# Kernel tuning notes

Measured on AMD Instinct MI355X. Metric: run time of the kernel, lower is better.

The kernel has to match this reference:

```python
import jax, jax.numpy as jnp
import numpy as np

B, S, D = 4, 512, 128


def setup_inputs() -> dict:
    key = jax.random.key(0)
    ks = jax.random.split(key, 9)
    scale = 1.0 / np.sqrt(D)
    return {
        "inputs": jax.random.normal(ks[0], (B, S, D), dtype=jnp.float32),
        "encoder_outputs": jax.random.normal(ks[1], (B, S, D), dtype=jnp.float32),
        "mask": jax.random.randint(ks[2], (B, S), 0, 2, dtype=jnp.int32),
        "W1": jax.random.uniform(ks[3], (D, D), jnp.float32, -scale, scale),
        "b1": jax.random.uniform(ks[4], (D,), jnp.float32, -scale, scale),
        "W2": jax.random.uniform(ks[5], (D, D), jnp.float32, -scale, scale),
        "b2": jax.random.uniform(ks[6], (D,), jnp.float32, -scale, scale),
        "v_w": jax.random.uniform(ks[7], (D,), jnp.float32, -scale, scale),
        "v_b": jax.random.uniform(ks[8], (1,), jnp.float32, -scale, scale),
    }


def reference(inputs, encoder_outputs, mask, W1, b1, W2, b2, v_w, v_b):
    # key_out: W1(encoder_outputs)  [B, S_k, D]
    key_out = jnp.einsum("bkd,de->bke", encoder_outputs, W1) + b1
    # query_out: W2(inputs)        [B, S_q, D]
    query_out = jnp.einsum("bqd,de->bqe", inputs, W2) + b2
    # additive attention, all query positions at once: [B, S_q, S_k, D]
    t = jnp.tanh(key_out[:, None, :, :] + query_out[:, :, None, :])
    ui = jnp.einsum("bqkd,d->bqk", t, v_w) + v_b[0]
    # mask out padded key positions for every query position
    valid = mask.astype(bool)[:, None, :]  # [B, 1, S_k]
    logits = jnp.where(valid, ui, -jnp.inf)
    preds = jnp.argmax(logits, axis=-1)
    return (logits, preds)
```

## Files before the change

kernel.cpp:

```cpp
#include <hip/hip_runtime.h>
#include <math.h>

#define NB 4
#define NS 512
#define ND 128

static constexpr float K2LE = 2.885390081777927f;

__device__ inline float fast_exp2(float x){
#if __has_builtin(__builtin_amdgcn_exp2f)
  return __builtin_amdgcn_exp2f(x);
#else
  float r; asm("v_exp_f32 %0, %1" : "=v"(r) : "v"(x)); return r;
#endif
}
__device__ inline float fast_rcp(float x){
#if __has_builtin(__builtin_amdgcn_rcpf)
  return __builtin_amdgcn_rcpf(x);
#else
  float r; asm("v_rcp_f32 %0, %1" : "=v"(r) : "v"(x)); return r;
#endif
}

__global__ void vw_reduce_kernel(const float* __restrict__ vw,
                                 const float* __restrict__ vb,
                                 float* __restrict__ Csum){
  __shared__ float sh[ND];
  int t = threadIdx.x;
  sh[t] = vw[t];
  __syncthreads();
  for (int s = ND/2; s > 0; s >>= 1){
    if (t < s) sh[t] += sh[t + s];
    __syncthreads();
  }
  if (t == 0) Csum[0] = sh[0] + vb[0];
}

__global__ __launch_bounds__(256) void proj_kernel(
    const float* __restrict__ inputs, const float* __restrict__ enc,
    const float* __restrict__ W1, const float* __restrict__ b1,
    const float* __restrict__ W2, const float* __restrict__ b2,
    const float* __restrict__ vw,
    float* __restrict__ EKT, float* __restrict__ RQ, float* __restrict__ WQ){
  const int ROWS = 8;
  int blk = blockIdx.x;
  bool is_key = (blk < (NB*NS)/ROWS);
  int rbase = (is_key ? blk : blk - (NB*NS)/ROWS) * ROWS;
  const float* X    = is_key ? enc : inputs;
  const float* W    = is_key ? W1  : W2;
  const float* bias = is_key ? b1  : b2;

  __shared__ float rows[ROWS][ND];
  {
    const float4* src = (const float4*)(X + (size_t)rbase*ND);
    float4* dst = (float4*)(&rows[0][0]);
    dst[threadIdx.x] = src[threadIdx.x];
  }
  __syncthreads();
  int rg = threadIdx.x >> 5;
  int ec = (threadIdx.x & 31) * 4;
  float4 acc = *(const float4*)(bias + ec);
  const float* rp = rows[rg];
  const float* wp = W + ec;
  #pragma unroll 8
  for (int d = 0; d < ND; ++d){
    float rv = rp[d];
    float4 w4 = *(const float4*)(wp + (size_t)d*ND);
    acc.x = fmaf(rv, w4.x, acc.x);
    acc.y = fmaf(rv, w4.y, acc.y);
    acc.z = fmaf(rv, w4.z, acc.z);
    acc.w = fmaf(rv, w4.w, acc.w);
  }
  int row = rbase + rg;
  if (is_key){
    int b = row >> 9, s = row & (NS-1);
    float* o = EKT + (size_t)b*ND*NS + s;
    o[(size_t)(ec+0)*NS] = fast_exp2(K2LE*acc.x);
    o[(size_t)(ec+1)*NS] = fast_exp2(K2LE*acc.y);
    o[(size_t)(ec+2)*NS] = fast_exp2(K2LE*acc.z);
    o[(size_t)(ec+3)*NS] = fast_exp2(K2LE*acc.w);
  } else {
    float4 vw4 = *(const float4*)(vw + ec);
    float4 r4, w4o;
    r4.x = fast_exp2(-K2LE*acc.x);
    r4.y = fast_exp2(-K2LE*acc.y);
    r4.z = fast_exp2(-K2LE*acc.z);
    r4.w = fast_exp2(-K2LE*acc.w);
    w4o.x = -2.0f*vw4.x*r4.x;
    w4o.y = -2.0f*vw4.y*r4.y;
    w4o.z = -2.0f*vw4.z*r4.z;
    w4o.w = -2.0f*vw4.w*r4.w;
    *(float4*)(RQ + (size_t)row*ND + ec) = r4;
    *(float4*)(WQ + (size_t)row*ND + ec) = w4o;
  }
}

__global__ __launch_bounds__(256) void score_kernel(
    const float* __restrict__ EKT, const float* __restrict__ RQ,
    const float* __restrict__ WQ, const int* __restrict__ mask,
    const float* __restrict__ Csum, float* __restrict__ out){
  int blk = blockIdx.x;
  int b = blk >> 7;
  int q0 = (blk & 127) * 4;
  int t = threadIdx.x;
  int k0 = t;
  const float* ek_b = EKT + (size_t)b*ND*NS;
  const float* rq0  = RQ + (size_t)(b*NS + q0)*ND;
  const float* wq0  = WQ + (size_t)(b*NS + q0)*ND;

  float acc[4][2];
  #pragma unroll
  for (int qi = 0; qi < 4; ++qi){ acc[qi][0] = 0.f; acc[qi][1] = 0.f; }

  for (int d = 0; d < ND; d += 4){
    float4 rq4[4], wq4[4];
    #pragma unroll
    for (int qi = 0; qi < 4; ++qi){
      rq4[qi] = *(const float4*)(rq0 + qi*ND + d);
      wq4[qi] = *(const float4*)(wq0 + qi*ND + d);
    }
    #pragma unroll
    for (int j = 0; j < 4; ++j){
      float ek0 = ek_b[(size_t)(d+j)*NS + k0];
      float ek1 = ek_b[(size_t)(d+j)*NS + k0 + 256];
      #pragma unroll
      for (int qi = 0; qi < 4; ++qi){
        float rq = ((const float*)&rq4[qi])[j];
        float wq = ((const float*)&wq4[qi])[j];
        acc[qi][0] = fmaf(wq, fast_rcp(ek0 + rq), acc[qi][0]);
        acc[qi][1] = fmaf(wq, fast_rcp(ek1 + rq), acc[qi][1]);
      }
    }
  }

  float C = Csum[0];
  int m0 = mask[b*NS + k0];
  int m1 = mask[b*NS + k0 + 256];
  const float NINF = -3.0e38f;

  float* logits = out;
  float* preds  = out + (size_t)NB*NS*NS;

  int lane = t & 63, wv = t >> 6;
  __shared__ float red_v[4][4];
  __shared__ int   red_i[4][4];

  #pragma unroll
  for (int qi = 0; qi < 4; ++qi){
    float u0 = m0 ? (C + acc[qi][0]) : NINF;
    float u1 = m1 ? (C + acc[qi][1]) : NINF;
    size_t base = (size_t)(b*NS + q0 + qi) * NS;
    logits[base + k0]       = u0;
    logits[base + k0 + 256] = u1;
    float bv = u0; int bi = k0;
    if (u1 > bv){ bv = u1; bi = k0 + 256; }
    #pragma unroll
    for (int off = 32; off > 0; off >>= 1){
      float ov = __shfl_down(bv, off);
      int   oi = __shfl_down(bi, off);
      if (ov > bv || (ov == bv && oi < bi)){ bv = ov; bi = oi; }
    }
    if (lane == 0){ red_v[wv][qi] = bv; red_i[wv][qi] = bi; }
  }
  __syncthreads();
  if (t < 4){
    float bv = red_v[0][t]; int bi = red_i[0][t];
    #pragma unroll
    for (int w = 1; w < 4; ++w){
      float ov = red_v[w][t]; int oi = red_i[w][t];
      if (ov > bv || (ov == bv && oi < bi)){ bv = ov; bi = oi; }
    }
    preds[b*NS + t + q0] = (float)bi;
  }
}

extern "C" void kernel_launch(void* const* d_in, const int* in_sizes, int n_in,
                              void* d_out, int out_size, void* d_ws, size_t ws_size,
                              hipStream_t stream){
  const float* inputs = (const float*)d_in[0];
  const float* enc    = (const float*)d_in[1];
  const int*   mask   = (const int*)d_in[2];
  const float* W1     = (const float*)d_in[3];
  const float* b1     = (const float*)d_in[4];
  const float* W2     = (const float*)d_in[5];
  const float* b2     = (const float*)d_in[6];
  const float* vw     = (const float*)d_in[7];
  const float* vb     = (const float*)d_in[8];
  float* out = (float*)d_out;

  float* ws  = (float*)d_ws;
  float* EKT = ws;
  float* RQ  = ws + 262144;
  float* WQ  = ws + 524288;
  float* Cs  = ws + 786432;

  vw_reduce_kernel<<<dim3(1),   dim3(128), 0, stream>>>(vw, vb, Cs);
  proj_kernel    <<<dim3(512),  dim3(256), 0, stream>>>(inputs, enc, W1, b1, W2, b2,
                                                        vw, EKT, RQ, WQ);
  score_kernel   <<<dim3(512),  dim3(256), 0, stream>>>(EKT, RQ, WQ, mask, Cs, out);
}
```

Baseline: 107.8 us.

## Fuse vw reduction into projection, transpose EKT via LDS, widen score blocks

Measured after the change: 105.1 us. 2.5% less time.

```diff
diff --git a/kernel.cpp b/kernel.cpp
--- a/kernel.cpp
+++ b/kernel.cpp
@@ -22,30 +22,29 @@
 #endif
 }
 
-__global__ void vw_reduce_kernel(const float* __restrict__ vw,
-                                 const float* __restrict__ vb,
-                                 float* __restrict__ Csum){
-  __shared__ float sh[ND];
-  int t = threadIdx.x;
-  sh[t] = vw[t];
-  __syncthreads();
-  for (int s = ND/2; s > 0; s >>= 1){
-    if (t < s) sh[t] += sh[t + s];
-    __syncthreads();
-  }
-  if (t == 0) Csum[0] = sh[0] + vb[0];
-}
-
 __global__ __launch_bounds__(256) void proj_kernel(
     const float* __restrict__ inputs, const float* __restrict__ enc,
     const float* __restrict__ W1, const float* __restrict__ b1,
     const float* __restrict__ W2, const float* __restrict__ b2,
-    const float* __restrict__ vw,
-    float* __restrict__ EKT, float* __restrict__ RQ, float* __restrict__ WQ){
-  const int ROWS = 8;
+    const float* __restrict__ vw, const float* __restrict__ vb,
+    float* __restrict__ EKT, float* __restrict__ RQ, float* __restrict__ WQ,
+    float* __restrict__ Csum){
+  const int ROWS = 16;
   int blk = blockIdx.x;
-  bool is_key = (blk < (NB*NS)/ROWS);
-  int rbase = (is_key ? blk : blk - (NB*NS)/ROWS) * ROWS;
+  int t = threadIdx.x;
+
+  if (blk == 256){
+    if (t < 64){
+      float v = vw[t] + vw[t + 64];
+      #pragma unroll
+      for (int off = 32; off; off >>= 1) v += __shfl_down(v, off);
+      if (t == 0) Csum[0] = v + vb[0];
+    }
+    return;
+  }
+
+  bool is_key = (blk < 128);
+  int rbase = (is_key ? blk : blk - 128) * ROWS;
   const float* X    = is_key ? enc : inputs;
   const float* W    = is_key ? W1  : W2;
   const float* bias = is_key ? b1  : b2;
@@ -54,123 +53,152 @@
   {
     const float4* src = (const float4*)(X + (size_t)rbase*ND);
     float4* dst = (float4*)(&rows[0][0]);
-    dst[threadIdx.x] = src[threadIdx.x];
+    dst[t]       = src[t];
+    dst[t + 256] = src[t + 256];
   }
   __syncthreads();
-  int rg = threadIdx.x >> 5;
-  int ec = (threadIdx.x & 31) * 4;
-  float4 acc = *(const float4*)(bias + ec);
-  const float* rp = rows[rg];
+
+  int rg = t >> 5;
+  int ec = (t & 31) * 4;
+  float4 b4 = *(const float4*)(bias + ec);
+  float4 acc0 = b4, acc1 = b4;
+  const float* r0 = rows[rg];
+  const float* r1 = rows[rg + 8];
   const float* wp = W + ec;
-  #pragma unroll 8
+  #pragma unroll 4
   for (int d = 0; d < ND; ++d){
-    float rv = rp[d];
     float4 w4 = *(const float4*)(wp + (size_t)d*ND);
-    acc.x = fmaf(rv, w4.x, acc.x);
-    acc.y = fmaf(rv, w4.y, acc.y);
-    acc.z = fmaf(rv, w4.z, acc.z);
-    acc.w = fmaf(rv, w4.w, acc.w);
-  }
-  int row = rbase + rg;
+    float a = r0[d], c = r1[d];
+    acc0.x = fmaf(a, w4.x, acc0.x);  acc1.x = fmaf(c, w4.x, acc1.x);
+    acc0.y = fmaf(a, w4.y, acc0.y);  acc1.y = fmaf(c, w4.y, acc1.y);
+    acc0.z = fmaf(a, w4.z, acc0.z);  acc1.z = fmaf(c, w4.z, acc1.z);
+    acc0.w = fmaf(a, w4.w, acc0.w);  acc1.w = fmaf(c, w4.w, acc1.w);
+  }
+
   if (is_key){
-    int b = row >> 9, s = row & (NS-1);
-    float* o = EKT + (size_t)b*ND*NS + s;
-    o[(size_t)(ec+0)*NS] = fast_exp2(K2LE*acc.x);
-    o[(size_t)(ec+1)*NS] = fast_exp2(K2LE*acc.y);
-    o[(size_t)(ec+2)*NS] = fast_exp2(K2LE*acc.z);
-    o[(size_t)(ec+3)*NS] = fast_exp2(K2LE*acc.w);
+    int b    = rbase >> 9;
+    int sloc = rbase & (NS - 1);
+    __syncthreads();
+    rows[rg][ec+0]   = fast_exp2(K2LE*acc0.x);
+    rows[rg][ec+1]   = fast_exp2(K2LE*acc0.y);
+    rows[rg][ec+2]   = fast_exp2(K2LE*acc0.z);
+    rows[rg][ec+3]   = fast_exp2(K2LE*acc0.w);
+    rows[rg+8][ec+0] = fast_exp2(K2LE*acc1.x);
+    rows[rg+8][ec+1] = fast_exp2(K2LE*acc1.y);
+    rows[rg+8][ec+2] = fast_exp2(K2LE*acc1.z);
+    rows[rg+8][ec+3] = fast_exp2(K2LE*acc1.w);
+    __syncthreads();
+    #pragma unroll
+    for (int rep = 0; rep < 2; ++rep){
+      int idx = t + rep*256;
+      int e  = idx >> 2;
+      int sc = (idx & 3) * 4;
+      float4 v = { rows[sc+0][e], rows[sc+1][e], rows[sc+2][e], rows[sc+3][e] };
+      *(float4*)(EKT + ((size_t)b*ND + e)*NS + sloc + sc) = v;
+    }
   } else {
+    int row0 = rbase + rg, row1 = row0 + 8;
     float4 vw4 = *(const float4*)(vw + ec);
-    float4 r4, w4o;
-    r4.x = fast_exp2(-K2LE*acc.x);
-    r4.y = fast_exp2(-K2LE*acc.y);
-    r4.z = fast_exp2(-K2LE*acc.z);
-    r4.w = fast_exp2(-K2LE*acc.w);
-    w4o.x = -2.0f*vw4.x*r4.x;
-    w4o.y = -2.0f*vw4.y*r4.y;
-    w4o.z = -2.0f*vw4.z*r4.z;
-    w4o.w = -2.0f*vw4.w*r4.w;
-    *(float4*)(RQ + (size_t)row*ND + ec) = r4;
-    *(float4*)(WQ + (size_t)row*ND + ec) = w4o;
-  }
-}
-
-__global__ __launch_bounds__(256) void score_kernel(
-    const float* __restrict__ EKT, const float* __restrict__ RQ,
-    const float* __restrict__ WQ, const int* __restrict__ mask,
+    float4 r4a, r4b, w4a, w4b;
+    r4a.x = fast_exp2(-K2LE*acc0.x);  r4b.x = fast_exp2(-K2LE*acc1.x);
+    r4a.y = fast_exp2(-K2LE*acc0.y);  r4b.y = fast_exp2(-K2LE*acc1.y);
+    r4a.z = fast_exp2(-K2LE*acc0.z);  r4b.z = fast_exp2(-K2LE*acc1.z);
+    r4a.w = fast_exp2(-K2LE*acc0.w);  r4b.w = fast_exp2(-K2LE*acc1.w);
+    w4a.x = -2.0f*vw4.x*r4a.x;  w4b.x = -2.0f*vw4.x*r4b.x;
+    w4a.y = -2.0f*vw4.y*r4a.y;  w4b.y = -2.0f*vw4.y*r4b.y;
+    w4a.z = -2.0f*vw4.z*r4a.z;  w4b.z = -2.0f*vw4.z*r4b.z;
+    w4a.w = -2.0f*vw4.w*r4a.w;  w4b.w = -2.0f*vw4.w*r4b.w;
+    *(float4*)(RQ + (size_t)row0*ND + ec) = r4a;
+    *(float4*)(WQ + (size_t)row0*ND + ec) = w4a;
+    *(float4*)(RQ + (size_t)row1*ND + ec) = r4b;
+    *(float4*)(WQ + (size_t)row1*ND + ec) = w4b;
+  }
+}
+
+__global__ __launch_bounds__(512) void score_kernel(
+    const float* __restrict__ EKT, const float* __restrict__ RQg,
+    const float* __restrict__ WQg, const int* __restrict__ mask,
     const float* __restrict__ Csum, float* __restrict__ out){
   int blk = blockIdx.x;
-  int b = blk >> 7;
+  int b  = blk >> 7;
   int q0 = (blk & 127) * 4;
-  int t = threadIdx.x;
-  int k0 = t;
-  const float* ek_b = EKT + (size_t)b*ND*NS;
-  const float* rq0  = RQ + (size_t)(b*NS + q0)*ND;
-  const float* wq0  = WQ + (size_t)(b*NS + q0)*ND;
-
-  float acc[4][2];
-  #pragma unroll
-  for (int qi = 0; qi < 4; ++qi){ acc[qi][0] = 0.f; acc[qi][1] = 0.f; }
-
+  int t  = threadIdx.x;
+
+  __shared__ float RQs[4*ND];
+  __shared__ float WQs[4*ND];
+  {
+    size_t base = (size_t)(b*NS + q0) * ND;
+    RQs[t] = RQg[base + t];
+    WQs[t] = WQg[base + t];
+  }
+  __syncthreads();
+
+  const float* ekp = EKT + (size_t)b*ND*NS + t;
+  float acc[4] = {0.f, 0.f, 0.f, 0.f};
+
+  #pragma unroll 2
   for (int d = 0; d < ND; d += 4){
     float4 rq4[4], wq4[4];
     #pragma unroll
     for (int qi = 0; qi < 4; ++qi){
-      rq4[qi] = *(const float4*)(rq0 + qi*ND + d);
-      wq4[qi] = *(const float4*)(wq0 + qi*ND + d);
-    }
-    #pragma unroll
-    for (int j = 0; j < 4; ++j){
-      float ek0 = ek_b[(size_t)(d+j)*NS + k0];
-      float ek1 = ek_b[(size_t)(d+j)*NS + k0 + 256];
-      #pragma unroll
-      for (int qi = 0; qi < 4; ++qi){
-        float rq = ((const float*)&rq4[qi])[j];
-        float wq = ((const float*)&wq4[qi])[j];
-        acc[qi][0] = fmaf(wq, fast_rcp(ek0 + rq), acc[qi][0]);
-        acc[qi][1] = fmaf(wq, fast_rcp(ek1 + rq), acc[qi][1]);
-      }
+      rq4[qi] = *(const float4*)&RQs[qi*ND + d];
+      wq4[qi] = *(const float4*)&WQs[qi*ND + d];
+    }
+    float ek0 = ekp[(size_t)(d+0)*NS];
+    float ek1 = ekp[(size_t)(d+1)*NS];
+    float ek2 = ekp[(size_t)(d+2)*NS];
+    float ek3 = ekp[(size_t)(d+3)*NS];
+    #pragma unroll
+    for (int qi = 0; qi < 4; ++qi){
+      const float* rqf = (const float*)&rq4[qi];
+      const float* wqf = (const float*)&wq4[qi];
+      acc[qi] = fmaf(wqf[0], fast_rcp(ek0 + rqf[0]), acc[qi]);
+      acc[qi] = fmaf(wqf[1], fast_rcp(ek1 + rqf[1]), acc[qi]);
+      acc[qi] = fmaf(wqf[2], fast_rcp(ek2 + rqf[2]), acc[qi]);
+      acc[qi] = fmaf(wqf[3], fast_rcp(ek3 + rqf[3]), acc[qi]);
     }
   }
 
   float C = Csum[0];
-  int m0 = mask[b*NS + k0];
-  int m1 = mask[b*NS + k0 + 256];
+  int m = mask[b*NS + t];
   const float NINF = -3.0e38f;
+  float u[4];
+  #pragma unroll
+  for (int qi = 0; qi < 4; ++qi) u[qi] = m ? (C + acc[qi]) : NINF;
 
   float* logits = out;
   float* preds  = out + (size_t)NB*NS*NS;
+  {
+    size_t base = (size_t)(b*NS + q0) * NS + t;
+    logits[base]        = u[0];
+    logits[base +   NS] = u[1];
+    logits[base + 2*NS] = u[2];
+    logits[base + 3*NS] = u[3];
+  }
 
   int lane = t & 63, wv = t >> 6;
-  __shared__ float red_v[4][4];
-  __shared__ int   red_i[4][4];
-
+  __shared__ float red_v[8][4];
+  __shared__ int   red_i[8][4];
   #pragma unroll
   for (int qi = 0; qi < 4; ++qi){
-    float u0 = m0 ? (C + acc[qi][0]) : NINF;
-    float u1 = m1 ? (C + acc[qi][1]) : NINF;
-    size_t base = (size_t)(b*NS + q0 + qi) * NS;
-    logits[base + k0]       = u0;
-    logits[base + k0 + 256] = u1;
-    float bv = u0; int bi = k0;
-    if (u1 > bv){ bv = u1; bi = k0 + 256; }
-    #pragma unroll
-    for (int off = 32; off > 0; off >>= 1){
-      float ov = __shfl_down(bv, off);
-      int   oi = __shfl_down(bi, off);
-      if (ov > bv || (ov == bv && oi < bi)){ bv = ov; bi = oi; }
-    }
-    if (lane == 0){ red_v[wv][qi] = bv; red_i[wv][qi] = bi; }
+    float v = u[qi]; int idx = t;
+    #pragma unroll
+    for (int off = 32; off; off >>= 1){
+      float ov = __shfl_down(v, off);
+      int   oi = __shfl_down(idx, off);
+      if (ov > v || (ov == v && oi < idx)){ v = ov; idx = oi; }
+    }
+    if (lane == 0){ red_v[wv][qi] = v; red_i[wv][qi] = idx; }
   }
   __syncthreads();
   if (t < 4){
-    float bv = red_v[0][t]; int bi = red_i[0][t];
-    #pragma unroll
-    for (int w = 1; w < 4; ++w){
+    float v = red_v[0][t]; int idx = red_i[0][t];
+    #pragma unroll
+    for (int w = 1; w < 8; ++w){
       float ov = red_v[w][t]; int oi = red_i[w][t];
-      if (ov > bv || (ov == bv && oi < bi)){ bv = ov; bi = oi; }
-    }
-    preds[b*NS + t + q0] = (float)bi;
+      if (ov > v || (ov == v && oi < idx)){ v = ov; idx = oi; }
+    }
+    preds[b*NS + q0 + t] = (float)idx;
   }
 }
 
@@ -194,8 +222,7 @@
   float* WQ  = ws + 524288;
   float* Cs  = ws + 786432;
 
-  vw_reduce_kernel<<<dim3(1),   dim3(128), 0, stream>>>(vw, vb, Cs);
-  proj_kernel    <<<dim3(512),  dim3(256), 0, stream>>>(inputs, enc, W1, b1, W2, b2,
-                                                        vw, EKT, RQ, WQ);
-  score_kernel   <<<dim3(512),  dim3(256), 0, stream>>>(EKT, RQ, WQ, mask, Cs, out);
-}
+  proj_kernel <<<dim3(257), dim3(256), 0, stream>>>(inputs, enc, W1, b1, W2, b2,
+                                                    vw, vb, EKT, RQ, WQ, Cs);
+  score_kernel<<<dim3(512), dim3(512), 0, stream>>>(EKT, RQ, WQ, mask, Cs, out);
+}
```
